# Kernel optimization log

Measured on AMD Instinct MI355X. Metric: run time of the kernel, lower is better.

Reference implementation:

```python
import jax, jax.numpy as jnp
import numpy as np

B, S, D, H = 2, 2048, 768, 12
DK = D // H
DF = 3072
SOFTCAP = 30.0
LN_EPS = 1e-5
NEG_INF = -1e30


def layer_norm(x, g, b):
    m = jnp.mean(x, axis=-1, keepdims=True)
    v = jnp.mean(jnp.square(x - m), axis=-1, keepdims=True)
    return (x - m) * jax.lax.rsqrt(v + LN_EPS) * g + b


def setup_inputs() -> dict:
    key = jax.random.key(0)
    ks = jax.random.split(key, 12)
    s = 0.02
    x = jax.random.normal(ks[0], (B, S, D), jnp.float32)
    count_bias = jax.random.normal(ks[1], (B, 1, S, S), jnp.float32)
    # causal mask: True = allowed
    attn_mask = jnp.broadcast_to(jnp.tril(jnp.ones((S, S), bool)), (B, 1, S, S))
    Wq = jax.random.normal(ks[2], (D, D), jnp.float32) * s
    Wk = jax.random.normal(ks[3], (D, D), jnp.float32) * s
    Wv = jax.random.normal(ks[4], (D, D), jnp.float32) * s
    Wo = jax.random.normal(ks[5], (D, D), jnp.float32) * s
    W1 = jax.random.normal(ks[6], (D, DF), jnp.float32) * s
    W2 = jax.random.normal(ks[7], (DF, D), jnp.float32) * s
    g1 = jnp.ones((D,), jnp.float32)
    b1 = jnp.zeros((D,), jnp.float32)
    g2 = jnp.ones((D,), jnp.float32)
    b2 = jnp.zeros((D,), jnp.float32)
    return dict(x=x, count_bias=count_bias, attn_mask=attn_mask, Wq=Wq, Wk=Wk,
                Wv=Wv, Wo=Wo, W1=W1, W2=W2, g1=g1, b1=b1, g2=g2, b2=b2)


def reference(x, count_bias, attn_mask, Wq, Wk, Wv, Wo, W1, W2, g1, b1, g2, b2):
    # pre-norm (note: residual taken from normed activations, faithful to source)
    h = layer_norm(x, g1, b1)                                   # (B,S,D)
    q = (h @ Wq).reshape(B, S, H, DK).transpose(0, 2, 1, 3)     # (B,H,S,DK)
    k = (h @ Wk).reshape(B, S, H, DK).transpose(0, 2, 1, 3)
    v = (h @ Wv).reshape(B, S, H, DK).transpose(0, 2, 1, 3)
    scale = 1.0 / np.sqrt(DK).astype(np.float32)
    scores = jnp.einsum('bhqd,bhkd->bhqk', q, k) * scale + count_bias
    scores = jnp.tanh(scores / SOFTCAP) * SOFTCAP               # softcap
    scores = jnp.where(attn_mask, scores, NEG_INF)
    weights = jax.nn.softmax(scores, axis=-1)
    o = jnp.einsum('bhqk,bhkd->bhqd', weights, v)               # (B,H,S,DK)
    o = o.transpose(0, 2, 1, 3).reshape(B, S, D) @ Wo
    x1 = o + h
    h2 = layer_norm(x1, g2, b2)
    ffn = jax.nn.gelu(h2 @ W1, approximate=False) @ W2
    return ffn + h2
```

## Files before the change

kernel.cpp:

```cpp
#include <hip/hip_runtime.h>
#include <hip/hip_bf16.h>
#include <cstdint>

#define Bn 2
#define Sn 2048
#define Dn 768
#define Hn 12
#define DKn 64
#define DFn 3072
#define Mrows 4096

typedef float f32x4 __attribute__((ext_vector_type(4)));
typedef __bf16 bf16x8 __attribute__((ext_vector_type(8)));
typedef short s16x8 __attribute__((ext_vector_type(8)));
typedef short s16x4 __attribute__((ext_vector_type(4)));

__device__ __forceinline__ f32x4 MFMA(s16x8 a, s16x8 b, f32x4 c) {
  return __builtin_amdgcn_mfma_f32_16x16x32_bf16(
      __builtin_bit_cast(bf16x8, a), __builtin_bit_cast(bf16x8, b), c, 0, 0, 0);
}

__device__ __forceinline__ void g2lds16(const void* g, void* l) {
  __builtin_amdgcn_global_load_lds(
      (__attribute__((address_space(1))) void*)(g),
      (__attribute__((address_space(3))) void*)(l), 16, 0, 0);
}

__device__ __forceinline__ short f2bf(float f) {
  unsigned u = __builtin_bit_cast(unsigned, f);
  unsigned r = (u + 0x7fffu + ((u >> 16) & 1u)) >> 16;
  return (short)r;
}

__device__ __forceinline__ float bf2f(short s) {
  unsigned u = ((unsigned)(unsigned short)s) << 16;
  return __builtin_bit_cast(float, u);
}

#define C1f 0.0120224586f
#define C2f 0.0961796722f
#define C3f -86.5617013f

__global__ __launch_bounds__(256) void bias_prep(const float* __restrict__ bias,
                                                 short* __restrict__ biasb) {
  int gid = blockIdx.x * 256 + threadIdx.x;
  size_t i8 = (size_t)gid * 8;
  int q = (int)((i8 >> 11) & 2047);
  int k0 = (int)(i8 & 2047);
  f32x4 v0 = *(const f32x4*)(bias + i8);
  f32x4 v1 = *(const f32x4*)(bias + i8 + 4);
  s16x8 o;
#pragma unroll
  for (int j = 0; j < 4; j++) o[j] = (k0 + j <= q) ? f2bf(v0[j] * C2f) : f2bf(-1e30f);
#pragma unroll
  for (int j = 0; j < 4; j++) o[4 + j] = (k0 + 4 + j <= q) ? f2bf(v1[j] * C2f) : f2bf(-1e30f);
  *(s16x8*)(biasb + i8) = o;
}

__global__ void wtrans(const float* __restrict__ in, short* __restrict__ out, int R, int C) {
  __shared__ float t[32][33];
  int c0 = blockIdx.x * 32, r0 = blockIdx.y * 32;
  int tx = threadIdx.x, ty = threadIdx.y;
#pragma unroll
  for (int i = 0; i < 4; i++) t[ty + i * 8][tx] = in[(size_t)(r0 + ty + i * 8) * C + c0 + tx];
  __syncthreads();
#pragma unroll
  for (int i = 0; i < 4; i++) out[(size_t)(c0 + ty + i * 8) * R + r0 + tx] = f2bf(t[tx][ty + i * 8]);
}

__global__ void wtrans3(const float* __restrict__ Wq, const float* __restrict__ Wk,
                        const float* __restrict__ Wv, short* __restrict__ out) {
  __shared__ float t[32][33];
  int z = blockIdx.z;
  const float* in = (z == 0) ? Wq : (z == 1) ? Wk : Wv;
  short* o = out + (size_t)z * Dn * Dn;
  int c0 = blockIdx.x * 32, r0 = blockIdx.y * 32;
  int tx = threadIdx.x, ty = threadIdx.y;
#pragma unroll
  for (int i = 0; i < 4; i++) t[ty + i * 8][tx] = in[(size_t)(r0 + ty + i * 8) * Dn + c0 + tx];
  __syncthreads();
#pragma unroll
  for (int i = 0; i < 4; i++) o[(size_t)(c0 + ty + i * 8) * Dn + r0 + tx] = f2bf(t[tx][ty + i * 8]);
}

__global__ __launch_bounds__(256) void ln_kernel(const float* __restrict__ x,
                                                 const float* __restrict__ g,
                                                 const float* __restrict__ b,
                                                 short* __restrict__ hb,
                                                 float* __restrict__ hf) {
  int row = blockIdx.x;
  const float* xr = x + (size_t)row * Dn;
  int tid = threadIdx.x;
  float v[3];
  float s = 0.f, ss = 0.f;
#pragma unroll
  for (int i = 0; i < 3; i++) {
    v[i] = xr[tid + i * 256];
    s += v[i];
    ss += v[i] * v[i];
  }
#pragma unroll
  for (int m = 1; m < 64; m <<= 1) {
    s += __shfl_xor(s, m);
    ss += __shfl_xor(ss, m);
  }
  __shared__ float red[8];
  int w = tid >> 6, lane = tid & 63;
  if (lane == 0) { red[w] = s; red[4 + w] = ss; }
  __syncthreads();
  s = red[0] + red[1] + red[2] + red[3];
  ss = red[4] + red[5] + red[6] + red[7];
  float mean = s * (1.0f / Dn);
  float var = ss * (1.0f / Dn) - mean * mean;
  float rs = rsqrtf(var + 1e-5f);
#pragma unroll
  for (int i = 0; i < 3; i++) {
    int c = tid + i * 256;
    float h = (v[i] - mean) * rs * g[c] + b[c];
    hb[(size_t)row * Dn + c] = f2bf(h);
    hf[(size_t)row * Dn + c] = h;
  }
}

template <int EPI>
__global__ __launch_bounds__(256, 2) void gemm_bt(const short* __restrict__ A,
                                                  const short* __restrict__ Bt,
                                                  short* __restrict__ Cb,
                                                  const float* __restrict__ addm,
                                                  float* __restrict__ Cf,
                                                  int M, int N, int K) {
  __shared__ __align__(16) short As[2][8192];
  __shared__ __align__(16) short Bs[2][8192];
  int tid = threadIdx.x, lane = tid & 63, w = tid >> 6, g = lane >> 4, lt = lane & 15;
  int wr = w >> 1, wc = w & 1;
  int m0 = blockIdx.x * 128, n0 = blockIdx.y * 128;
  int r0 = tid >> 3, c8 = tid & 7;
  const short* Ags[4];
  const short* Bgs[4];
#pragma unroll
  for (int h = 0; h < 4; h++) {
    int row = h * 32 + r0;
    int cc = c8 ^ (row & 7);
    Ags[h] = A + (size_t)(m0 + row) * K + cc * 8;
    Bgs[h] = Bt + (size_t)(n0 + row) * K + cc * 8;
  }
  int sw = lt & 7;
  int ch0 = (g ^ sw) * 8, ch1 = ((4 + g) ^ sw) * 8;
  f32x4 acc[4][4] = {};
#pragma unroll
  for (int h = 0; h < 4; h++) {
    g2lds16(Ags[h], &As[0][(h * 256 + tid) * 8]);
    g2lds16(Bgs[h], &Bs[0][(h * 256 + tid) * 8]);
  }
  __syncthreads();
  int nsteps = K >> 6;
  for (int t = 0; t < nsteps; t++) {
    int cur = t & 1;
    if (t + 1 < nsteps) {
      int k0 = (t + 1) << 6;
#pragma unroll
      for (int h = 0; h < 4; h++) {
        g2lds16(Ags[h] + k0, &As[cur ^ 1][(h * 256 + tid) * 8]);
        g2lds16(Bgs[h] + k0, &Bs[cur ^ 1][(h * 256 + tid) * 8]);
      }
    }
    s16x8 af[4][2], bf[4][2];
#pragma unroll
    for (int i = 0; i < 4; i++) {
      int row = wr * 64 + i * 16 + lt;
      af[i][0] = *(const s16x8*)&As[cur][row * 64 + ch0];
      af[i][1] = *(const s16x8*)&As[cur][row * 64 + ch1];
    }
#pragma unroll
    for (int i = 0; i < 4; i++) {
      int row = wc * 64 + i * 16 + lt;
      bf[i][0] = *(const s16x8*)&Bs[cur][row * 64 + ch0];
      bf[i][1] = *(const s16x8*)&Bs[cur][row * 64 + ch1];
    }
#pragma unroll
    for (int mi = 0; mi < 4; mi++)
#pragma unroll
      for (int ni = 0; ni < 4; ni++) {
        acc[mi][ni] = MFMA(af[mi][0], bf[ni][0], acc[mi][ni]);
        acc[mi][ni] = MFMA(af[mi][1], bf[ni][1], acc[mi][ni]);
      }
    __syncthreads();
  }
#pragma unroll
  for (int mi = 0; mi < 4; mi++) {
    int m = m0 + wr * 64 + mi * 16 + g * 4;
#pragma unroll
    for (int ni = 0; ni < 4; ni++) {
      int n = n0 + wc * 64 + ni * 16 + lt;
#pragma unroll
      for (int r = 0; r < 4; r++) {
        float v = acc[mi][ni][r];
        size_t idx = (size_t)(m + r) * N + n;
        if constexpr (EPI == 0) {
          Cb[idx] = f2bf(v);
        } else if constexpr (EPI == 1) {
          float ge = 0.5f * v * (1.0f + erff(v * 0.70710678f));
          Cb[idx] = f2bf(ge);
        } else {
          Cf[idx] = v + addm[idx];
        }
      }
    }
  }
}

template <int EPI>
__global__ __launch_bounds__(256, 4) void gemm64(const short* __restrict__ A,
                                                 const short* __restrict__ Bt,
                                                 short* __restrict__ Cb,
                                                 const float* __restrict__ addm,
                                                 float* __restrict__ Cf,
                                                 int M, int N, int K) {
  __shared__ __align__(16) short As[2][4096];
  __shared__ __align__(16) short Bs[2][4096];
  int tid = threadIdx.x, lane = tid & 63, w = tid >> 6, g = lane >> 4, lt = lane & 15;
  int wr = w >> 1, wc = w & 1;
  int m0 = blockIdx.x * 64, n0 = blockIdx.y * 64;
  int r0 = tid >> 3, cc = (tid & 7) ^ (r0 & 7);
  const short* asrc0 = A + (size_t)(m0 + r0) * K + cc * 8;
  const short* asrc1 = A + (size_t)(m0 + r0 + 32) * K + cc * 8;
  const short* bsrc0 = Bt + (size_t)(n0 + r0) * K + cc * 8;
  const short* bsrc1 = Bt + (size_t)(n0 + r0 + 32) * K + cc * 8;
  int sw = lt & 7;
  int ch0 = (g ^ sw) * 8, ch1 = ((4 + g) ^ sw) * 8;
  f32x4 acc[2][2] = {};
  g2lds16(asrc0, &As[0][tid * 8]);
  g2lds16(asrc1, &As[0][2048 + tid * 8]);
  g2lds16(bsrc0, &Bs[0][tid * 8]);
  g2lds16(bsrc1, &Bs[0][2048 + tid * 8]);
  __syncthreads();
  int nsteps = K >> 6;
  for (int t = 0; t < nsteps; t++) {
    int cur = t & 1;
    if (t + 1 < nsteps) {
      int k0 = (t + 1) << 6;
      g2lds16(asrc0 + k0, &As[cur ^ 1][tid * 8]);
      g2lds16(asrc1 + k0, &As[cur ^ 1][2048 + tid * 8]);
      g2lds16(bsrc0 + k0, &Bs[cur ^ 1][tid * 8]);
      g2lds16(bsrc1 + k0, &Bs[cur ^ 1][2048 + tid * 8]);
    }
    s16x8 af[2][2], bf[2][2];
#pragma unroll
    for (int mi = 0; mi < 2; mi++) {
      af[mi][0] = *(const s16x8*)&As[cur][(wr * 32 + mi * 16 + lt) * 64 + ch0];
      af[mi][1] = *(const s16x8*)&As[cur][(wr * 32 + mi * 16 + lt) * 64 + ch1];
    }
#pragma unroll
    for (int ni = 0; ni < 2; ni++) {
      bf[ni][0] = *(const s16x8*)&Bs[cur][(wc * 32 + ni * 16 + lt) * 64 + ch0];
      bf[ni][1] = *(const s16x8*)&Bs[cur][(wc * 32 + ni * 16 + lt) * 64 + ch1];
    }
#pragma unroll
    for (int mi = 0; mi < 2; mi++)
#pragma unroll
      for (int ni = 0; ni < 2; ni++) {
        acc[mi][ni] = MFMA(af[mi][0], bf[ni][0], acc[mi][ni]);
        acc[mi][ni] = MFMA(af[mi][1], bf[ni][1], acc[mi][ni]);
      }
    __syncthreads();
  }
#pragma unroll
  for (int mi = 0; mi < 2; mi++) {
    int m = m0 + wr * 32 + mi * 16 + g * 4;
#pragma unroll
    for (int ni = 0; ni < 2; ni++) {
      int n = n0 + wc * 32 + ni * 16 + lt;
#pragma unroll
      for (int r = 0; r < 4; r++) {
        float v = acc[mi][ni][r];
        size_t idx = (size_t)(m + r) * N + n;
        if constexpr (EPI == 0) {
          Cb[idx] = f2bf(v);
        } else if constexpr (EPI == 1) {
          float ge = 0.5f * v * (1.0f + erff(v * 0.70710678f));
          Cb[idx] = f2bf(ge);
        } else {
          Cf[idx] = v + addm[idx];
        }
      }
    }
  }
}

__global__ void vtrans(const short* __restrict__ qkv, short* __restrict__ vt) {
  __shared__ short t[32][33];
  int bh = blockIdx.z;
  int b = bh / Hn, h = bh % Hn;
  int s0 = blockIdx.x * 32, d0 = blockIdx.y * 32;
  int tx = threadIdx.x, ty = threadIdx.y;
#pragma unroll
  for (int i = 0; i < 4; i++)
    t[ty + i * 8][tx] =
        qkv[(size_t)(b * Sn + s0 + ty + i * 8) * (3 * Dn) + 2 * Dn + h * DKn + d0 + tx];
  __syncthreads();
#pragma unroll
  for (int i = 0; i < 4; i++)
    vt[(size_t)(bh * DKn + d0 + ty + i * 8) * Sn + s0 + tx] = t[tx][ty + i * 8];
}

__global__ __launch_bounds__(256, 3) void attn_kernel(const short* __restrict__ qkv,
                                                      const short* __restrict__ vt,
                                                      const short* __restrict__ biasb,
                                                      short* __restrict__ o) {
  __shared__ __align__(16) short Ks[2][4096];
  __shared__ __align__(16) short Vs[2][4096];
  __shared__ __align__(16) short plds[4][16][72];
  int bh = blockIdx.x;
  int by = blockIdx.y;
  int qt = (by & 1) ? (31 - (by >> 1)) : (by >> 1);
  int b = bh / Hn, h = bh - b * Hn;
  int tid = threadIdx.x, w = tid >> 6, lane = tid & 63, g = lane >> 4, lt = lane & 15;
  int q0 = qt * 64 + w * 16;
  const short* qbase = qkv + (size_t)(b * Sn + q0 + lt) * (3 * Dn) + h * DKn;
  s16x8 qf0 = *(const s16x8*)(qbase + g * 8);
  s16x8 qf1 = *(const s16x8*)(qbase + 32 + g * 8);
  int sr0 = tid >> 3, scc = (tid & 7) ^ (sr0 & 7);
  const short* kseg = qkv + (size_t)b * Sn * (3 * Dn) + Dn + h * DKn;
  const short* ksrc0 = kseg + (size_t)sr0 * (3 * Dn) + scc * 8;
  const short* ksrc1 = kseg + (size_t)(sr0 + 32) * (3 * Dn) + scc * 8;
  const short* vseg = vt + (size_t)bh * DKn * Sn;
  const short* vsrc0 = vseg + (size_t)sr0 * Sn + scc * 8;
  const short* vsrc1 = vseg + (size_t)(sr0 + 32) * Sn + scc * 8;
  int sw = lt & 7;
  int ch0 = (g ^ sw) * 8, ch1 = ((4 + g) ^ sw) * 8;
  const short* bbase = biasb + ((size_t)b * Sn + q0 + g * 4) * Sn + lt;
  f32x4 oacc[4] = {};
  float lsum[4] = {0.f, 0.f, 0.f, 0.f};
  g2lds16(ksrc0, &Ks[0][tid * 8]);
  g2lds16(ksrc1, &Ks[0][2048 + tid * 8]);
  g2lds16(vsrc0, &Vs[0][tid * 8]);
  g2lds16(vsrc1, &Vs[0][2048 + tid * 8]);
  short sb[16];
#pragma unroll
  for (int c = 0; c < 4; c++)
#pragma unroll
    for (int r = 0; r < 4; r++) sb[c * 4 + r] = bbase[(size_t)r * Sn + c * 16];
  __syncthreads();
  for (int t = 0; t <= qt; t++) {
    int cur = t & 1;
    int kc0 = t * 64;
    if (t < qt) {
      size_t koff = (size_t)(kc0 + 64) * (3 * Dn);
      g2lds16(ksrc0 + koff, &Ks[cur ^ 1][tid * 8]);
      g2lds16(ksrc1 + koff, &Ks[cur ^ 1][2048 + tid * 8]);
      g2lds16(vsrc0 + kc0 + 64, &Vs[cur ^ 1][tid * 8]);
      g2lds16(vsrc1 + kc0 + 64, &Vs[cur ^ 1][2048 + tid * 8]);
    }
    short sbn[16];
    if (t < qt) {
      int kn = kc0 + 64;
#pragma unroll
      for (int c = 0; c < 4; c++)
#pragma unroll
        for (int r = 0; r < 4; r++) sbn[c * 4 + r] = bbase[(size_t)r * Sn + kn + c * 16];
    }
    s16x8 kf[4][2];
#pragma unroll
    for (int c = 0; c < 4; c++) {
      kf[c][0] = *(const s16x8*)&Ks[cur][(c * 16 + lt) * 64 + ch0];
      kf[c][1] = *(const s16x8*)&Ks[cur][(c * 16 + lt) * 64 + ch1];
    }
    f32x4 s[4] = {};
#pragma unroll
    for (int c = 0; c < 4; c++) {
      s[c] = MFMA(qf0, kf[c][0], s[c]);
      s[c] = MFMA(qf1, kf[c][1], s[c]);
    }
    s16x8 vf[4][2];
#pragma unroll
    for (int dt = 0; dt < 4; dt++) {
      vf[dt][0] = *(const s16x8*)&Vs[cur][(dt * 16 + lt) * 64 + ch0];
      vf[dt][1] = *(const s16x8*)&Vs[cur][(dt * 16 + lt) * 64 + ch1];
    }
#pragma unroll
    for (int c = 0; c < 4; c++) {
#pragma unroll
      for (int r = 0; r < 4; r++) {
        float targ = fmaf(s[c][r], C1f, bf2f(sb[c * 4 + r]));
        float e = __builtin_amdgcn_exp2f(targ);
        float u = __builtin_amdgcn_rcpf(1.0f + e);
        float p = __builtin_amdgcn_exp2f(C3f * u);
        lsum[r] += p;
        plds[w][g * 4 + r][c * 16 + lt] = f2bf(p);
      }
    }
    s16x8 pf0 = *(const s16x8*)&plds[w][lt][g * 8];
    s16x8 pf1 = *(const s16x8*)&plds[w][lt][32 + g * 8];
#pragma unroll
    for (int dt = 0; dt < 4; dt++) {
      oacc[dt] = MFMA(pf0, vf[dt][0], oacc[dt]);
      oacc[dt] = MFMA(pf1, vf[dt][1], oacc[dt]);
    }
    __syncthreads();
    if (t < qt) {
#pragma unroll
      for (int i = 0; i < 16; i++) sb[i] = sbn[i];
    }
  }
  float inv[4];
#pragma unroll
  for (int r = 0; r < 4; r++) {
    float l = lsum[r];
    l += __shfl_xor(l, 1);
    l += __shfl_xor(l, 2);
    l += __shfl_xor(l, 4);
    l += __shfl_xor(l, 8);
    inv[r] = __builtin_amdgcn_rcpf(l);
  }
  short* obase = o + (size_t)(b * Sn + q0 + g * 4) * Dn + h * DKn + lt;
#pragma unroll
  for (int dt = 0; dt < 4; dt++)
#pragma unroll
    for (int r = 0; r < 4; r++) obase[(size_t)r * Dn + dt * 16] = f2bf(oacc[dt][r] * inv[r]);
}

extern "C" void kernel_launch(void* const* d_in, const int* in_sizes, int n_in,
                              void* d_out, int out_size, void* d_ws, size_t ws_size,
                              hipStream_t stream) {
  const float* x = (const float*)d_in[0];
  const float* bias = (const float*)d_in[1];
  const float* Wq = (const float*)d_in[3];
  const float* Wk = (const float*)d_in[4];
  const float* Wv = (const float*)d_in[5];
  const float* Wo = (const float*)d_in[6];
  const float* W1 = (const float*)d_in[7];
  const float* W2 = (const float*)d_in[8];
  const float* g1 = (const float*)d_in[9];
  const float* b1 = (const float*)d_in[10];
  const float* g2 = (const float*)d_in[11];
  const float* b2 = (const float*)d_in[12];
  float* out = (float*)d_out;
  char* ws = (char*)d_ws;

  short* wqkv_t = (short*)(ws + 0);
  short* wo_t = (short*)(ws + 3538944);
  short* w1_t = (short*)(ws + 4718592);
  short* w2_t = (short*)(ws + 9437184);
  short* hb = (short*)(ws + 14155776);
  float* hf = (float*)(ws + 20447232);
  short* qkv = (short*)(ws + 33030144);
  short* a1 = qkv;
  short* vt = (short*)(ws + 58195968);
  float* x1 = (float*)(ws + 58195968);
  short* o_ = (short*)(ws + 70778880);
  short* biasb = (short*)(ws + 77070336);
  short* h2b = hb;
  float* h2f = hf;

  dim3 tb(32, 8);
  bias_prep<<<4096, 256, 0, stream>>>(bias, biasb);
  wtrans3<<<dim3(24, 24, 3), tb, 0, stream>>>(Wq, Wk, Wv, wqkv_t);
  wtrans<<<dim3(24, 24), tb, 0, stream>>>(Wo, wo_t, Dn, Dn);
  wtrans<<<dim3(96, 24), tb, 0, stream>>>(W1, w1_t, Dn, DFn);
  wtrans<<<dim3(24, 96), tb, 0, stream>>>(W2, w2_t, DFn, Dn);

  ln_kernel<<<Mrows, 256, 0, stream>>>(x, g1, b1, hb, hf);

  gemm_bt<0><<<dim3(32, 18), 256, 0, stream>>>(hb, wqkv_t, qkv, nullptr, nullptr,
                                               Mrows, 3 * Dn, Dn);
  vtrans<<<dim3(64, 2, Bn * Hn), tb, 0, stream>>>(qkv, vt);
  attn_kernel<<<dim3(24, 32), 256, 0, stream>>>(qkv, vt, biasb, o_);

  gemm64<2><<<dim3(64, 12), 256, 0, stream>>>(o_, wo_t, nullptr, hf, x1,
                                              Mrows, Dn, Dn);
  ln_kernel<<<Mrows, 256, 0, stream>>>(x1, g2, b2, h2b, h2f);
  gemm_bt<1><<<dim3(32, 24), 256, 0, stream>>>(h2b, w1_t, a1, nullptr, nullptr,
                                               Mrows, DFn, Dn);
  gemm64<2><<<dim3(64, 12), 256, 0, stream>>>(a1, w2_t, nullptr, h2f, out,
                                              Mrows, Dn, DFn);
}
```

Before: 339.9 us.

## Simplify GEMM to single-buffered K=32 tiles and enlarge attention blocks to 128 queries

The bf16 GEMM drops double-buffered 64-wide K tiles in favor of single-buffered 32-wide tiles with a new swizzle and two barriers per step. This halves LDS use and raises potential occupancy, but loses the overlap of global loads with MFMA work. The attention kernel now uses 512-thread blocks covering 128 query rows, so each K/V tile loaded into LDS is shared by 8 waves. It also drops the balanced causal tile ordering for a simple descending order.

```diff
diff --git a/kernel.cpp b/kernel.cpp
--- a/kernel.cpp
+++ b/kernel.cpp
@@ -123,67 +123,43 @@
 }
 
 template <int EPI>
-__global__ __launch_bounds__(256, 2) void gemm_bt(const short* __restrict__ A,
-                                                  const short* __restrict__ Bt,
-                                                  short* __restrict__ Cb,
-                                                  const float* __restrict__ addm,
-                                                  float* __restrict__ Cf,
-                                                  int M, int N, int K) {
-  __shared__ __align__(16) short As[2][8192];
-  __shared__ __align__(16) short Bs[2][8192];
-  int tid = threadIdx.x, lane = tid & 63, w = tid >> 6, g = lane >> 4, lt = lane & 15;
+__global__ __launch_bounds__(256) void gemm_bt(const short* __restrict__ A,
+                                               const short* __restrict__ Bt,
+                                               short* __restrict__ Cb,
+                                               const float* __restrict__ addm,
+                                               float* __restrict__ Cf,
+                                               int M, int N, int K) {
+  __shared__ __align__(16) short As[4096];
+  __shared__ __align__(16) short Bs[4096];
+  int tid = threadIdx.x;
+  int lane = tid & 63, w = tid >> 6, g = lane >> 4, lt = lane & 15;
   int wr = w >> 1, wc = w & 1;
   int m0 = blockIdx.x * 128, n0 = blockIdx.y * 128;
-  int r0 = tid >> 3, c8 = tid & 7;
-  const short* Ags[4];
-  const short* Bgs[4];
-#pragma unroll
-  for (int h = 0; h < 4; h++) {
-    int row = h * 32 + r0;
-    int cc = c8 ^ (row & 7);
-    Ags[h] = A + (size_t)(m0 + row) * K + cc * 8;
-    Bgs[h] = Bt + (size_t)(n0 + row) * K + cc * 8;
-  }
-  int sw = lt & 7;
-  int ch0 = (g ^ sw) * 8, ch1 = ((4 + g) ^ sw) * 8;
+  int r0 = tid >> 2, c4 = tid & 3;
+  int cc = c4 ^ ((r0 >> 1) & 3);
+  const short* Ag0 = A + (size_t)(m0 + r0) * K + cc * 8;
+  const short* Ag1 = A + (size_t)(m0 + r0 + 64) * K + cc * 8;
+  const short* Bg0 = Bt + (size_t)(n0 + r0) * K + cc * 8;
+  const short* Bg1 = Bt + (size_t)(n0 + r0 + 64) * K + cc * 8;
+  int swr = (lt >> 1) & 3;
+  int cfrag = (g ^ swr) * 8;
   f32x4 acc[4][4] = {};
-#pragma unroll
-  for (int h = 0; h < 4; h++) {
-    g2lds16(Ags[h], &As[0][(h * 256 + tid) * 8]);
-    g2lds16(Bgs[h], &Bs[0][(h * 256 + tid) * 8]);
-  }
-  __syncthreads();
-  int nsteps = K >> 6;
-  for (int t = 0; t < nsteps; t++) {
-    int cur = t & 1;
-    if (t + 1 < nsteps) {
-      int k0 = (t + 1) << 6;
-#pragma unroll
-      for (int h = 0; h < 4; h++) {
-        g2lds16(Ags[h] + k0, &As[cur ^ 1][(h * 256 + tid) * 8]);
-        g2lds16(Bgs[h] + k0, &Bs[cur ^ 1][(h * 256 + tid) * 8]);
-      }
-    }
-    s16x8 af[4][2], bf[4][2];
+  for (int k0 = 0; k0 < K; k0 += 32) {
+    g2lds16(Ag0 + k0, &As[tid * 8]);
+    g2lds16(Ag1 + k0, &As[2048 + tid * 8]);
+    g2lds16(Bg0 + k0, &Bs[tid * 8]);
+    g2lds16(Bg1 + k0, &Bs[2048 + tid * 8]);
+    __syncthreads();
+    s16x8 af[4], bfr[4];
 #pragma unroll
     for (int i = 0; i < 4; i++) {
-      int row = wr * 64 + i * 16 + lt;
-      af[i][0] = *(const s16x8*)&As[cur][row * 64 + ch0];
-      af[i][1] = *(const s16x8*)&As[cur][row * 64 + ch1];
-    }
-#pragma unroll
-    for (int i = 0; i < 4; i++) {
-      int row = wc * 64 + i * 16 + lt;
-      bf[i][0] = *(const s16x8*)&Bs[cur][row * 64 + ch0];
-      bf[i][1] = *(const s16x8*)&Bs[cur][row * 64 + ch1];
+      af[i] = *(const s16x8*)&As[(wr * 64 + i * 16 + lt) * 32 + cfrag];
+      bfr[i] = *(const s16x8*)&Bs[(wc * 64 + i * 16 + lt) * 32 + cfrag];
     }
 #pragma unroll
     for (int mi = 0; mi < 4; mi++)
 #pragma unroll
-      for (int ni = 0; ni < 4; ni++) {
-        acc[mi][ni] = MFMA(af[mi][0], bf[ni][0], acc[mi][ni]);
-        acc[mi][ni] = MFMA(af[mi][1], bf[ni][1], acc[mi][ni]);
-      }
+      for (int ni = 0; ni < 4; ni++) acc[mi][ni] = MFMA(af[mi], bfr[ni], acc[mi][ni]);
     __syncthreads();
   }
 #pragma unroll
@@ -303,56 +279,47 @@
     vt[(size_t)(bh * DKn + d0 + ty + i * 8) * Sn + s0 + tx] = t[tx][ty + i * 8];
 }
 
-__global__ __launch_bounds__(256, 3) void attn_kernel(const short* __restrict__ qkv,
+__global__ __launch_bounds__(512, 2) void attn_kernel(const short* __restrict__ qkv,
                                                       const short* __restrict__ vt,
                                                       const short* __restrict__ biasb,
                                                       short* __restrict__ o) {
   __shared__ __align__(16) short Ks[2][4096];
   __shared__ __align__(16) short Vs[2][4096];
-  __shared__ __align__(16) short plds[4][16][72];
+  __shared__ __align__(16) short plds[8][16][72];
   int bh = blockIdx.x;
-  int by = blockIdx.y;
-  int qt = (by & 1) ? (31 - (by >> 1)) : (by >> 1);
+  int qt = 15 - (int)blockIdx.y;
   int b = bh / Hn, h = bh - b * Hn;
   int tid = threadIdx.x, w = tid >> 6, lane = tid & 63, g = lane >> 4, lt = lane & 15;
-  int q0 = qt * 64 + w * 16;
+  int q0 = qt * 128 + w * 16;
   const short* qbase = qkv + (size_t)(b * Sn + q0 + lt) * (3 * Dn) + h * DKn;
   s16x8 qf0 = *(const s16x8*)(qbase + g * 8);
   s16x8 qf1 = *(const s16x8*)(qbase + 32 + g * 8);
-  int sr0 = tid >> 3, scc = (tid & 7) ^ (sr0 & 7);
-  const short* kseg = qkv + (size_t)b * Sn * (3 * Dn) + Dn + h * DKn;
-  const short* ksrc0 = kseg + (size_t)sr0 * (3 * Dn) + scc * 8;
-  const short* ksrc1 = kseg + (size_t)(sr0 + 32) * (3 * Dn) + scc * 8;
-  const short* vseg = vt + (size_t)bh * DKn * Sn;
-  const short* vsrc0 = vseg + (size_t)sr0 * Sn + scc * 8;
-  const short* vsrc1 = vseg + (size_t)(sr0 + 32) * Sn + scc * 8;
+  int srow = tid >> 3, scc = (tid & 7) ^ (srow & 7);
+  const short* ksrc = qkv + (size_t)(b * Sn + srow) * (3 * Dn) + Dn + h * DKn + scc * 8;
+  const short* vsrc = vt + ((size_t)bh * DKn + srow) * Sn + scc * 8;
   int sw = lt & 7;
   int ch0 = (g ^ sw) * 8, ch1 = ((4 + g) ^ sw) * 8;
   const short* bbase = biasb + ((size_t)b * Sn + q0 + g * 4) * Sn + lt;
   f32x4 oacc[4] = {};
   float lsum[4] = {0.f, 0.f, 0.f, 0.f};
-  g2lds16(ksrc0, &Ks[0][tid * 8]);
-  g2lds16(ksrc1, &Ks[0][2048 + tid * 8]);
-  g2lds16(vsrc0, &Vs[0][tid * 8]);
-  g2lds16(vsrc1, &Vs[0][2048 + tid * 8]);
+  g2lds16(ksrc, &Ks[0][tid * 8]);
+  g2lds16(vsrc, &Vs[0][tid * 8]);
   short sb[16];
 #pragma unroll
   for (int c = 0; c < 4; c++)
 #pragma unroll
     for (int r = 0; r < 4; r++) sb[c * 4 + r] = bbase[(size_t)r * Sn + c * 16];
   __syncthreads();
-  for (int t = 0; t <= qt; t++) {
+  int nt = 2 * qt + 2;
+  for (int t = 0; t < nt; t++) {
     int cur = t & 1;
     int kc0 = t * 64;
-    if (t < qt) {
-      size_t koff = (size_t)(kc0 + 64) * (3 * Dn);
-      g2lds16(ksrc0 + koff, &Ks[cur ^ 1][tid * 8]);
-      g2lds16(ksrc1 + koff, &Ks[cur ^ 1][2048 + tid * 8]);
-      g2lds16(vsrc0 + kc0 + 64, &Vs[cur ^ 1][tid * 8]);
-      g2lds16(vsrc1 + kc0 + 64, &Vs[cur ^ 1][2048 + tid * 8]);
+    if (t + 1 < nt) {
+      g2lds16(ksrc + (size_t)(kc0 + 64) * (3 * Dn), &Ks[cur ^ 1][tid * 8]);
+      g2lds16(vsrc + kc0 + 64, &Vs[cur ^ 1][tid * 8]);
     }
     short sbn[16];
-    if (t < qt) {
+    if (t + 1 < nt) {
       int kn = kc0 + 64;
 #pragma unroll
       for (int c = 0; c < 4; c++)
@@ -397,7 +364,7 @@
       oacc[dt] = MFMA(pf1, vf[dt][1], oacc[dt]);
     }
     __syncthreads();
-    if (t < qt) {
+    if (t + 1 < nt) {
 #pragma unroll
       for (int i = 0; i < 16; i++) sb[i] = sbn[i];
     }
@@ -464,7 +431,7 @@
   gemm_bt<0><<<dim3(32, 18), 256, 0, stream>>>(hb, wqkv_t, qkv, nullptr, nullptr,
                                                Mrows, 3 * Dn, Dn);
   vtrans<<<dim3(64, 2, Bn * Hn), tb, 0, stream>>>(qkv, vt);
-  attn_kernel<<<dim3(24, 32), 256, 0, stream>>>(qkv, vt, biasb, o_);
+  attn_kernel<<<dim3(24, 16), 512, 0, stream>>>(qkv, vt, biasb, o_);
 
   gemm64<2><<<dim3(64, 12), 256, 0, stream>>>(o_, wo_t, nullptr, hf, x1,
                                               Mrows, Dn, Dn);
```

New measurement: 339.0 us. No clear change (-0.3%).
